# Kernel optimization log

Hardware: AMD Instinct MI355X
Metric: run time of the kernel (lower is better)

The kernel has to match this reference:

```python
import jax, jax.numpy as jnp
import numpy as np

# Sizes derived from init_kwargs via calc_mlp_features:
# total_param=2117777, router_ratio=0.002 -> router_param=4235.554, expert_param=264192
# expert_hidden = 256, router_hidden = 352
N = 131072      # number of coordinate points
CIN = 3         # expert_insize == router_insize (xyz coords)
E = 8           # num_experts
K = 2           # top_k
H = 256         # expert_hidden (also SIREN data_channel)
RH = 352        # router_hidden
NHID = 3        # expert_layers - 2 hidden SIREN layers
W0C = 30.0      # sine frequency w0


def setup_inputs() -> dict:
    key = jax.random.key(0)
    ks = jax.random.split(key, 16)
    u = lambda k, shape, a: jax.random.uniform(k, shape, jnp.float32, -a, a)
    x = jax.random.uniform(ks[0], (N, CIN), jnp.float32, -1.0, 1.0)
    context = jax.random.uniform(ks[1], (N, CIN), jnp.float32, -1.0, 1.0)
    # Router: kaiming-normal weights, torch-default uniform biases
    Wr1 = jax.random.normal(ks[2], (CIN, RH), jnp.float32) * np.float32(np.sqrt(2.0 / CIN))
    br1 = u(ks[3], (RH,), 1.0 / np.sqrt(CIN))
    Wr2 = jax.random.normal(ks[4], (RH, E), jnp.float32) * np.float32(np.sqrt(2.0 / RH))
    br2 = u(ks[5], (E,), 1.0 / np.sqrt(RH))
    # SIREN experts (stacked over E): first layer U(-1/in, 1/in), rest U(+-sqrt(6/in)/30)
    sb = np.sqrt(6.0 / H) / 30.0
    W0 = u(ks[6], (E, CIN, H), 1.0 / CIN)
    b0 = u(ks[7], (E, H), 1.0 / np.sqrt(CIN))
    Wh = u(ks[8], (E, NHID, H, H), sb)
    bh = u(ks[9], (E, NHID, H), 1.0 / np.sqrt(H))
    Wo = u(ks[10], (E, H, H), sb)
    bo = u(ks[11], (E, H), 1.0 / np.sqrt(H))
    # Decoder: Linear(H,H)+ReLU+Linear(H,1)
    Wd1 = jax.random.normal(ks[12], (H, H), jnp.float32) * np.float32(np.sqrt(2.0 / H))
    bd1 = u(ks[13], (H,), 1.0 / np.sqrt(H))
    Wd2 = jax.random.normal(ks[14], (H, 1), jnp.float32) * np.float32(np.sqrt(2.0 / H))
    bd2 = u(ks[15], (1,), 1.0 / np.sqrt(H))
    return dict(x=x, context=context, Wr1=Wr1, br1=br1, Wr2=Wr2, br2=br2,
                W0=W0, b0=b0, Wh=Wh, bh=bh, Wo=Wo, bo=bo,
                Wd1=Wd1, bd1=bd1, Wd2=Wd2, bd2=bd2)


def reference(x, context, Wr1, br1, Wr2, br2, W0, b0, Wh, bh, Wo, bo, Wd1, bd1, Wd2, bd2):
    n = x.shape[0]
    # --- NoisyTopkRouter (eval path: no noise) ---
    logits = jnp.maximum(context @ Wr1 + br1, 0.0) @ Wr2 + br2          # [N, E]
    topv, topi = jax.lax.top_k(logits, K)                                # [N, K]
    # softmax over -inf-filled sparse logits == softmax over the top-k values
    w = jax.nn.softmax(topv, axis=-1)                                    # [N, K]
    gating = jnp.zeros_like(logits).at[jnp.arange(n)[:, None], topi].set(w)  # [N, E], zero off top-k
    # --- Per-expert SIREN, weighted combine ---
    # Masked dispatch + scatter-add in the original equals dense weighted sum
    # because gating is exactly zero for non-selected experts.
    def expert_step(acc, p):
        W0e, b0e, Whe, bhe, Woe, boe, ge = p
        h = jnp.sin(W0C * (x @ W0e + b0e))                # [N, H]
        for i in range(NHID):
            h = jnp.sin(W0C * (h @ Whe[i] + bhe[i]))
        out = h @ Woe + boe                               # [N, H], no output activation
        return acc + out * ge[:, None], None
    acc0 = jnp.zeros((n, H), dtype=x.dtype)
    final, _ = jax.lax.scan(expert_step, acc0, (W0, b0, Wh, bh, Wo, bo, gating.T))
    # --- Decoder ---
    return jnp.maximum(final @ Wd1 + bd1, 0.0) @ Wd2 + bd2               # [N, 1]
```

## Files before the change

kernel.cpp:

```cpp
#include <hip/hip_runtime.h>
#include <stdint.h>

#define N_PTS 131072
#define RH    352
#define BM    256
#define BME   128
#define TPB   512
#define SREV  4.774648292756860f

typedef short  bf16x8 __attribute__((ext_vector_type(8)));
typedef float  f32x16 __attribute__((ext_vector_type(16)));

__device__ __forceinline__ unsigned short f2bf(float f) {
  uint32_t u = __builtin_bit_cast(uint32_t, f);
  u = (u + 0x7FFFu + ((u >> 16) & 1u)) >> 16;
  return (unsigned short)u;
}
__device__ __forceinline__ float bf2f(unsigned short s) {
  return __builtin_bit_cast(float, ((uint32_t)s) << 16);
}
__device__ __forceinline__ float vsin1(float x) {
  float xf = x - floorf(x);
  float r;
  asm("v_sin_f32 %0, %1" : "=v"(r) : "v"(xf));
  return r;
}
__device__ __forceinline__ void ldsload16(const void* g, void* ldsWaveBase) {
  typedef __attribute__((address_space(3))) uint8_t lds_b;
  typedef __attribute__((address_space(1))) uint8_t glob_b;
  __builtin_amdgcn_global_load_lds((const glob_b*)g, (lds_b*)ldsWaveBase, 16, 0, 0);
}
__device__ __forceinline__ f32x16 mfma_bf16(bf16x8 a, bf16x8 b, f32x16 c) {
  return __builtin_amdgcn_mfma_f32_32x32x16_bf16(a, b, c, 0, 0, 0);
}

__global__ __launch_bounds__(512) void pack_kernel(
    const float* __restrict__ W0, const float* __restrict__ b0,
    const float* __restrict__ Wh, const float* __restrict__ bh,
    const float* __restrict__ Wo, const float* __restrict__ bo,
    const float* __restrict__ Wd1, const float* __restrict__ bd1,
    short* __restrict__ pW0, short* __restrict__ pWh,
    short* __restrict__ pWo, short* __restrict__ pWd1)
{
  int b = blockIdx.x, tid = threadIdx.x;
  int jb = tid >> 6, l = tid & 63;
  int j  = jb*32 + (l & 31);
  int s0 = (l >> 5) * 8;
  unsigned short o[8];
  short* dp;

  if (b < 544) {
    int m = b / 17, slice = b % 17;
    int e = m >> 2, t = m & 3;
    const float* src; const float* bias; float scale; short* dst;
    if (t < 3) { src = Wh + (size_t)(e*3+t)*65536; bias = bh + (size_t)(e*3+t)*256; scale = SREV; dst = pWh + (size_t)(e*3+t)*69632; }
    else       { src = Wo + (size_t)e*65536;       bias = bo + (size_t)e*256;       scale = 1.0f; dst = pWo + (size_t)e*69632; }
    if (slice < 16) {
      #pragma unroll
      for (int i = 0; i < 8; ++i) {
        int k = slice*16 + s0 + i;
        o[i] = f2bf(scale * src[(size_t)k*256 + j]);
      }
    } else {
      #pragma unroll
      for (int i = 0; i < 8; ++i) o[i] = 0;
      if (s0 == 0) {
        float a = scale * bias[j];
        unsigned short h = f2bf(a);
        o[0] = h; o[1] = f2bf(a - bf2f(h));
      }
    }
    dp = dst + (size_t)slice*4096 + jb*512 + l*8;
  } else if (b < 552) {
    int e = b - 544;
    const float* w0 = W0 + (size_t)e*768;
    const float* bb = b0 + (size_t)e*256;
    #pragma unroll
    for (int i = 0; i < 8; ++i) {
      int s = s0 + i;
      unsigned short v = 0;
      if (s < 3) v = f2bf(SREV * w0[(size_t)s*256 + j]);
      else if (s < 6) { float a = SREV * w0[(size_t)(s-3)*256 + j]; unsigned short h = f2bf(a); v = f2bf(a - bf2f(h)); }
      else if (s < 9) v = f2bf(SREV * w0[(size_t)(s-6)*256 + j]);
      else if (s == 9)  v = f2bf(SREV * bb[j]);
      else if (s == 10) { float a = SREV * bb[j]; unsigned short h = f2bf(a); v = f2bf(a - bf2f(h)); }
      o[i] = v;
    }
    dp = pW0 + (size_t)e*4096 + jb*512 + l*8;
  } else {
    int slice = b - 552;
    if (slice < 16) {
      #pragma unroll
      for (int i = 0; i < 8; ++i) {
        int k = slice*16 + s0 + i;
        o[i] = f2bf(Wd1[(size_t)k*256 + j]);
      }
    } else {
      #pragma unroll
      for (int i = 0; i < 8; ++i) o[i] = 0;
      if (s0 == 0) {
        float a = bd1[j];
        unsigned short h = f2bf(a);
        o[0] = h; o[1] = f2bf(a - bf2f(h));
      }
    }
    dp = pWd1 + (size_t)slice*4096 + jb*512 + l*8;
  }
  uint4 v;
  v.x = (uint32_t)o[0] | ((uint32_t)o[1] << 16);
  v.y = (uint32_t)o[2] | ((uint32_t)o[3] << 16);
  v.z = (uint32_t)o[4] | ((uint32_t)o[5] << 16);
  v.w = (uint32_t)o[6] | ((uint32_t)o[7] << 16);
  *(uint4*)dp = v;
}

__global__ __launch_bounds__(256) void router_kernel(
    const float* __restrict__ ctx, const float* __restrict__ Wr1,
    const float* __restrict__ br1, const float* __restrict__ Wr2,
    const float* __restrict__ br2, uint4* __restrict__ topk,
    uint32_t* __restrict__ counts)
{
  __shared__ double w1d[RH*4];
  __shared__ double w2d[RH*8];
  __shared__ uint32_t lcnt[8];
  int tid = threadIdx.x;
  for (int i = tid; i < RH; i += 256) {
    w1d[i*4+0] = (double)Wr1[i];
    w1d[i*4+1] = (double)Wr1[352 + i];
    w1d[i*4+2] = (double)Wr1[704 + i];
    w1d[i*4+3] = (double)br1[i];
  }
  for (int i = tid; i < RH*8; i += 256) w2d[i] = (double)Wr2[i];
  if (tid < 8) lcnt[tid] = 0;
  __syncthreads();

  int n = blockIdx.x*256 + tid;
  double c0 = (double)ctx[(size_t)n*3+0];
  double c1 = (double)ctx[(size_t)n*3+1];
  double c2 = (double)ctx[(size_t)n*3+2];
  double lg[8];
  #pragma unroll
  for (int e = 0; e < 8; ++e) lg[e] = (double)br2[e];
  for (int j = 0; j < RH; ++j) {
    const double* a = &w1d[j*4];
    double h = c0*a[0] + c1*a[1] + c2*a[2] + a[3];
    h = h > 0.0 ? h : 0.0;
    const double* bq = &w2d[j*8];
    lg[0] += h*bq[0]; lg[1] += h*bq[1]; lg[2] += h*bq[2]; lg[3] += h*bq[3];
    lg[4] += h*bq[4]; lg[5] += h*bq[5]; lg[6] += h*bq[6]; lg[7] += h*bq[7];
  }
  double v0 = -1e300, v1 = -1e300; int i0 = 0, i1 = 0;
  #pragma unroll
  for (int e = 0; e < 8; ++e) {
    double lv = lg[e];
    if (lv > v0)      { v1 = v0; i1 = i0; v0 = lv; i0 = e; }
    else if (lv > v1) { v1 = lv; i1 = e; }
  }
  float ex = __expf((float)(v1 - v0));
  float s = 1.0f / (1.0f + ex);
  uint4 t;
  t.x = (uint32_t)i0 | ((uint32_t)i1 << 8);
  t.y = __builtin_bit_cast(uint32_t, s);
  t.z = __builtin_bit_cast(uint32_t, ex * s);
  t.w = 0;
  topk[n] = t;
  atomicAdd(&lcnt[i0], 1u); atomicAdd(&lcnt[i1], 1u);
  __syncthreads();
  if (tid < 8) atomicAdd(&counts[tid], lcnt[tid]);
}

__global__ void scan_kernel(const uint32_t* __restrict__ counts,
                            uint32_t* __restrict__ offsets,
                            uint32_t* __restrict__ cursors)
{
  if (threadIdx.x == 0) {
    uint32_t o = 0;
    for (int e = 0; e < 8; ++e) { offsets[e] = o; cursors[e] = o; o += counts[e]; }
    offsets[8] = o;
  }
}

__global__ __launch_bounds__(256) void scatter_kernel(
    const uint4* __restrict__ topk, uint32_t* __restrict__ cursors,
    uint32_t* __restrict__ plist, float* __restrict__ pw)
{
  __shared__ uint32_t lc[8], lb[8];
  int tid = threadIdx.x;
  if (tid < 8) lc[tid] = 0;
  __syncthreads();
  int n = blockIdx.x*256 + tid;
  uint4 t = topk[n];
  uint32_t e0 = t.x & 255u, e1 = (t.x >> 8) & 255u;
  uint32_t p0 = atomicAdd(&lc[e0], 1u);
  uint32_t p1 = atomicAdd(&lc[e1], 1u);
  __syncthreads();
  if (tid < 8) lb[tid] = atomicAdd(&cursors[tid], lc[tid]);
  __syncthreads();
  uint32_t d0 = lb[e0] + p0, d1 = lb[e1] + p1;
  plist[d0] = ((uint32_t)n << 1);      pw[d0] = __builtin_bit_cast(float, t.y);
  plist[d1] = ((uint32_t)n << 1) | 1u; pw[d1] = __builtin_bit_cast(float, t.z);
}

#define LDS_EXPERT 81920

__global__ __launch_bounds__(TPB, 4) void expert_kernel(
    const float* __restrict__ x, const uint32_t* __restrict__ counts,
    const uint32_t* __restrict__ offsets, const uint32_t* __restrict__ plist,
    const float* __restrict__ pw, const short* __restrict__ pW0,
    const short* __restrict__ pWh, const short* __restrict__ pWo,
    short* __restrict__ outbuf)
{
  extern __shared__ __align__(16) uint8_t smem[];
  uint8_t* hB = smem;
  uint8_t* wB = smem + 65536;

  int tid = threadIdx.x;
  int lane = tid & 63;
  int wv = tid >> 6;
  int nw = wv & 1;
  int jw = wv >> 1;

  int b = blockIdx.x;
  int e = 0; uint32_t cnt = 0;
  for (; e < 8; ++e) {
    cnt = counts[e];
    int nt = (int)((cnt + (BME-1)) / BME);
    if (b < nt) break;
    b -= nt;
  }
  if (e >= 8) return;
  uint32_t base = offsets[e] + (uint32_t)b * BME;
  int nvalid = (int)cnt - b*BME; if (nvalid > BME) nvalid = BME;

  float wgt[2];
  #pragma unroll
  for (int c = 0; c < 2; ++c) {
    int n = (nw*2 + c)*32 + (lane & 31);
    wgt[c] = (n < nvalid) ? pw[base + n] : 0.0f;
  }
  int rr = tid >> 2;
  int rq = tid & 3;
  uint32_t psv = (rr < nvalid) ? plist[base + rr] : 0u;

  ldsload16((const uint8_t*)(pW0 + (size_t)e*4096) + (size_t)tid*16,
            wB + wv*1024);
  if (tid < BME) {
    float x0 = 0.0f, x1 = 0.0f, x2 = 0.0f;
    if (tid < nvalid) {
      uint32_t v = plist[base + tid];
      const float* xp = x + (size_t)(v >> 1)*3;
      x0 = xp[0]; x1 = xp[1]; x2 = xp[2];
    }
    unsigned short h0 = f2bf(x0), h1 = f2bf(x1), h2 = f2bf(x2);
    unsigned short l0 = f2bf(x0 - bf2f(h0)), l1 = f2bf(x1 - bf2f(h1)), l2 = f2bf(x2 - bf2f(h2));
    uint4 r0, r1;
    r0.x = (uint32_t)h0 | ((uint32_t)h1 << 16);
    r0.y = (uint32_t)h2 | ((uint32_t)h0 << 16);
    r0.z = (uint32_t)h1 | ((uint32_t)h2 << 16);
    r0.w = (uint32_t)l0 | ((uint32_t)l1 << 16);
    r1.x = (uint32_t)l2 | (0x3F80u << 16);
    r1.y = 0x3F80u;
    r1.z = 0u; r1.w = 0u;
    uint4* dst = (uint4*)(wB + 8192 + tid*32);
    dst[0] = r0; dst[1] = r1;
  }
  __syncthreads();

  f32x16 acc[2][2];
  #pragma unroll
  for (int a2 = 0; a2 < 2; ++a2)
    #pragma unroll
    for (int c = 0; c < 2; ++c)
      #pragma unroll
      for (int r = 0; r < 16; ++r) acc[a2][c][r] = 0.0f;

  {
    bf16x8 av[2], bv[2];
    #pragma unroll
    for (int a2 = 0; a2 < 2; ++a2)
      av[a2] = *(const bf16x8*)(wB + (jw*2 + a2)*1024 + lane*16);
    #pragma unroll
    for (int c = 0; c < 2; ++c) {
      int n = (nw*2 + c)*32 + (lane & 31);
      bv[c] = *(const bf16x8*)(wB + 8192 + n*32 + ((lane >> 5)*16));
    }
    #pragma unroll
    for (int a2 = 0; a2 < 2; ++a2)
      #pragma unroll
      for (int c = 0; c < 2; ++c)
        acc[a2][c] = mfma_bf16(av[a2], bv[c], acc[a2][c]);
  }
  __syncthreads();

  #pragma unroll
  for (int a2 = 0; a2 < 2; ++a2) {
    int jb = jw*2 + a2;
    #pragma unroll
    for (int c = 0; c < 2; ++c) {
      int n = (nw*2 + c)*32 + (lane & 31);
      uint32_t rowb = (uint32_t)n * 512u;
      uint32_t sw = (uint32_t)((n & 7) << 4);
      #pragma unroll
      for (int g = 0; g < 4; ++g) {
        float s0f = vsin1(acc[a2][c][g*4+0]);
        float s1f = vsin1(acc[a2][c][g*4+1]);
        float s2f = vsin1(acc[a2][c][g*4+2]);
        float s3f = vsin1(acc[a2][c][g*4+3]);
        uint2 pv;
        pv.x = (uint32_t)f2bf(s0f) | ((uint32_t)f2bf(s1f) << 16);
        pv.y = (uint32_t)f2bf(s2f) | ((uint32_t)f2bf(s3f) << 16);
        int j0 = jb*32 + g*8 + ((lane >> 5) << 2);
        uint32_t off = (rowb + (uint32_t)(j0*2)) ^ sw;
        *(uint2*)(hB + off) = pv;
      }
    }
  }
  ldsload16((const uint8_t*)(pWh + (size_t)e*3*69632) + (size_t)tid*16,
            wB + wv*1024);
  __syncthreads();

  const short* mats[4];
  mats[0] = pWh + (size_t)(e*3+0)*69632;
  mats[1] = pWh + (size_t)(e*3+1)*69632;
  mats[2] = pWh + (size_t)(e*3+2)*69632;
  mats[3] = pWo + (size_t)e*69632;

  bf16x8 bbias;
  #pragma unroll
  for (int i = 0; i < 8; ++i) bbias[i] = 0;
  if (lane < 32) { bbias[0] = (short)0x3F80; bbias[1] = (short)0x3F80; }

  #pragma unroll 1
  for (int L = 0; L < 4; ++L) {
    const short* Wsrc = mats[L];
    #pragma unroll
    for (int a2 = 0; a2 < 2; ++a2)
      #pragma unroll
      for (int c = 0; c < 2; ++c)
        #pragma unroll
        for (int r = 0; r < 16; ++r) acc[a2][c][r] = 0.0f;
    #pragma unroll 1
    for (int kb = 0; kb < 17; ++kb) {
      if (kb < 16)
        ldsload16((const uint8_t*)(Wsrc + (size_t)(kb+1)*4096) + (size_t)tid*16,
                  wB + ((kb+1) & 1)*8192 + wv*1024);
      const uint8_t* wcur = wB + (kb & 1)*8192;
      bf16x8 av[2];
      #pragma unroll
      for (int a2 = 0; a2 < 2; ++a2)
        av[a2] = *(const bf16x8*)(wcur + (jw*2 + a2)*1024 + lane*16);
      bf16x8 bv[2];
      if (kb < 16) {
        #pragma unroll
        for (int c = 0; c < 2; ++c) {
          int n = (nw*2 + c)*32 + (lane & 31);
          uint32_t off = ((uint32_t)n*512u + (uint32_t)kb*32u + (uint32_t)((lane >> 5)*16))
                         ^ (uint32_t)((n & 7) << 4);
          bv[c] = *(const bf16x8*)(hB + off);
        }
      } else {
        bv[0] = bbias; bv[1] = bbias;
      }
      #pragma unroll
      for (int a2 = 0; a2 < 2; ++a2)
        #pragma unroll
        for (int c = 0; c < 2; ++c)
          acc[a2][c] = mfma_bf16(av[a2], bv[c], acc[a2][c]);
      __syncthreads();
    }
    if (L < 3) {
      #pragma unroll
      for (int a2 = 0; a2 < 2; ++a2) {
        int jb = jw*2 + a2;
        #pragma unroll
        for (int c = 0; c < 2; ++c) {
          int n = (nw*2 + c)*32 + (lane & 31);
          uint32_t rowb = (uint32_t)n * 512u;
          uint32_t sw = (uint32_t)((n & 7) << 4);
          #pragma unroll
          for (int g = 0; g < 4; ++g) {
            float s0f = vsin1(acc[a2][c][g*4+0]);
            float s1f = vsin1(acc[a2][c][g*4+1]);
            float s2f = vsin1(acc[a2][c][g*4+2]);
            float s3f = vsin1(acc[a2][c][g*4+3]);
            uint2 pv;
            pv.x = (uint32_t)f2bf(s0f) | ((uint32_t)f2bf(s1f) << 16);
            pv.y = (uint32_t)f2bf(s2f) | ((uint32_t)f2bf(s3f) << 16);
            int j0 = jb*32 + g*8 + ((lane >> 5) << 2);
            uint32_t off = (rowb + (uint32_t)(j0*2)) ^ sw;
            *(uint2*)(hB + off) = pv;
          }
        }
      }
      ldsload16((const uint8_t*)mats[L+1] + (size_t)tid*16, wB + wv*1024);
      __syncthreads();
    }
  }

  #pragma unroll
  for (int a2 = 0; a2 < 2; ++a2) {
    int jb = jw*2 + a2;
    #pragma unroll
    for (int c = 0; c < 2; ++c) {
      int n = (nw*2 + c)*32 + (lane & 31);
      float w = wgt[c];
      uint32_t rowb = (uint32_t)n * 512u;
      uint32_t sw = (uint32_t)((n & 7) << 4);
      #pragma unroll
      for (int g = 0; g < 4; ++g) {
        float s0f = acc[a2][c][g*4+0] * w;
        float s1f = acc[a2][c][g*4+1] * w;
        float s2f = acc[a2][c][g*4+2] * w;
        float s3f = acc[a2][c][g*4+3] * w;
        uint2 pv;
        pv.x = (uint32_t)f2bf(s0f) | ((uint32_t)f2bf(s1f) << 16);
        pv.y = (uint32_t)f2bf(s2f) | ((uint32_t)f2bf(s3f) << 16);
        int j0 = jb*32 + g*8 + ((lane >> 5) << 2);
        uint32_t off = (rowb + (uint32_t)(j0*2)) ^ sw;
        *(uint2*)(hB + off) = pv;
      }
    }
  }
  __syncthreads();
  if (rr < nvalid) {
    uint4* dst = (uint4*)(outbuf + ((size_t)(psv & 1)*N_PTS + (size_t)(psv >> 1))*256 + rq*64);
    uint32_t rowb = (uint32_t)rr*512u + (uint32_t)rq*128u;
    uint32_t sw = (uint32_t)((rr & 7) << 4);
    #pragma unroll
    for (int c = 0; c < 8; ++c)
      dst[c] = *(const uint4*)(hB + ((rowb + (uint32_t)c*16u) ^ sw));
  }
}

#define LDS_DEC 150528

__global__ __launch_bounds__(TPB, 2) void decoder_kernel(
    const short* __restrict__ outbuf, const short* __restrict__ pWd1,
    const float* __restrict__ Wd2v, const float* __restrict__ bd2,
    float* __restrict__ outp)
{
  extern __shared__ __align__(16) uint8_t smem[];
  uint8_t* hB = smem;
  uint8_t* wB = smem + 131072;
  float* wd2 = (float*)(smem + 147456);
  float* part = (float*)(smem + 148480);

  int tid = threadIdx.x;
  int lane = tid & 63;
  int wv = tid >> 6;
  int nw = wv & 3;
  int jw = wv >> 2;
  int tbase = blockIdx.x * BM;

  ldsload16((const uint8_t*)pWd1 + (size_t)tid*16, wB + (tid >> 6)*1024);
  if (tid < 256) wd2[tid] = Wd2v[tid];

  const short* o0 = outbuf + (size_t)tbase*256;
  const short* o1 = outbuf + ((size_t)N_PTS + tbase)*256;
  #pragma unroll 1
  for (int it = 0; it < 16; ++it) {
    int c = it*512 + tid;
    uint4 a  = *(const uint4*)(o0 + (size_t)c*8);
    uint4 bq = *(const uint4*)(o1 + (size_t)c*8);
    uint4 ov;
    uint32_t* ap = (uint32_t*)&a;
    uint32_t* bp = (uint32_t*)&bq;
    uint32_t* op = (uint32_t*)&ov;
    #pragma unroll
    for (int w = 0; w < 4; ++w) {
      uint32_t ua = ap[w], ub = bp[w];
      float f0 = bf2f((unsigned short)(ua & 0xFFFFu)) + bf2f((unsigned short)(ub & 0xFFFFu));
      float f1 = bf2f((unsigned short)(ua >> 16))     + bf2f((unsigned short)(ub >> 16));
      op[w] = (uint32_t)f2bf(f0) | ((uint32_t)f2bf(f1) << 16);
    }
    int n = c >> 5;
    uint32_t off = ((uint32_t)n*512u + (uint32_t)(c & 31)*16u) ^ (uint32_t)((n & 7) << 4);
    *(uint4*)(hB + off) = ov;
  }
  __syncthreads();

  f32x16 acc[4][2];
  #pragma unroll
  for (int a2 = 0; a2 < 4; ++a2)
    #pragma unroll
    for (int c = 0; c < 2; ++c)
      #pragma unroll
      for (int r = 0; r < 16; ++r) acc[a2][c][r] = 0.0f;
  bf16x8 bbias;
  #pragma unroll
  for (int i = 0; i < 8; ++i) bbias[i] = 0;
  if (lane < 32) { bbias[0] = (short)0x3F80; bbias[1] = (short)0x3F80; }

  #pragma unroll 1
  for (int kb = 0; kb < 17; ++kb) {
    if (kb < 16)
      ldsload16((const uint8_t*)(pWd1 + (size_t)(kb+1)*4096) + (size_t)tid*16,
                wB + ((kb+1) & 1)*8192 + (tid >> 6)*1024);
    const uint8_t* wcur = wB + (kb & 1)*8192;
    bf16x8 av[4];
    #pragma unroll
    for (int a2 = 0; a2 < 4; ++a2)
      av[a2] = *(const bf16x8*)(wcur + (jw*4 + a2)*1024 + lane*16);
    bf16x8 bv[2];
    if (kb < 16) {
      #pragma unroll
      for (int c = 0; c < 2; ++c) {
        int n = (nw*2 + c)*32 + (lane & 31);
        uint32_t off = ((uint32_t)n*512u + (uint32_t)kb*32u + (uint32_t)((lane >> 5)*16))
                       ^ (uint32_t)((n & 7) << 4);
        bv[c] = *(const bf16x8*)(hB + off);
      }
    } else {
      bv[0] = bbias; bv[1] = bbias;
    }
    #pragma unroll
    for (int a2 = 0; a2 < 4; ++a2)
      #pragma unroll
      for (int c = 0; c < 2; ++c)
        acc[a2][c] = mfma_bf16(av[a2], bv[c], acc[a2][c]);
    __syncthreads();
  }

  float p0 = 0.0f, p1 = 0.0f;
  #pragma unroll
  for (int a2 = 0; a2 < 4; ++a2) {
    int jb = jw*4 + a2;
    #pragma unroll
    for (int c = 0; c < 2; ++c) {
      #pragma unroll
      for (int r = 0; r < 16; ++r) {
        int j = jb*32 + (r & 3) + ((r >> 2) << 3) + ((lane >> 5) << 2);
        float v = acc[a2][c][r];
        v = v > 0.0f ? v : 0.0f;
        float t = v * wd2[j];
        if (c == 0) p0 += t; else p1 += t;
      }
    }
  }
  p0 += __shfl_xor(p0, 32);
  p1 += __shfl_xor(p1, 32);
  if (lane < 32) {
    part[jw*256 + (nw*2+0)*32 + lane] = p0;
    part[jw*256 + (nw*2+1)*32 + lane] = p1;
  }
  __syncthreads();
  if (tid < 256)
    outp[tbase + tid] = part[tid] + part[256 + tid] + bd2[0];
}

extern "C" void kernel_launch(void* const* d_in, const int* in_sizes, int n_in,
                              void* d_out, int out_size, void* d_ws, size_t ws_size,
                              hipStream_t stream) {
  const float* x   = (const float*)d_in[0];
  const float* ctx = (const float*)d_in[1];
  const float* Wr1 = (const float*)d_in[2];
  const float* br1 = (const float*)d_in[3];
  const float* Wr2 = (const float*)d_in[4];
  const float* br2 = (const float*)d_in[5];
  const float* W0  = (const float*)d_in[6];
  const float* b0  = (const float*)d_in[7];
  const float* Wh  = (const float*)d_in[8];
  const float* bh  = (const float*)d_in[9];
  const float* Wo  = (const float*)d_in[10];
  const float* bo  = (const float*)d_in[11];
  const float* Wd1 = (const float*)d_in[12];
  const float* bd1 = (const float*)d_in[13];
  const float* Wd2 = (const float*)d_in[14];
  const float* bd2 = (const float*)d_in[15];
  float* out = (float*)d_out;

  const size_t WS_COUNTS  = 0;
  const size_t WS_CURSORS = 256;
  const size_t WS_OFFSETS = 512;
  const size_t WS_TOPK    = 1024;
  const size_t WS_PLIST   = WS_TOPK  + (size_t)N_PTS*16;
  const size_t WS_PW      = WS_PLIST + (size_t)N_PTS*8;
  const size_t WS_PW0     = WS_PW    + (size_t)N_PTS*8;
  const size_t WS_PWH     = WS_PW0   + (size_t)8*8192;
  const size_t WS_PWO     = WS_PWH   + (size_t)24*139264;
  const size_t WS_PWD1    = WS_PWO   + (size_t)8*139264;
  const size_t WS_OUT     = WS_PWD1  + (size_t)139264;
  const size_t WS_END     = WS_OUT   + (size_t)2*N_PTS*256*2;

  if (ws_size < WS_END) {
    hipMemsetAsync(d_out, 0xFF, (size_t)out_size*4, stream);
    return;
  }

  uint8_t* ws = (uint8_t*)d_ws;
  uint32_t* counts  = (uint32_t*)(ws + WS_COUNTS);
  uint32_t* cursors = (uint32_t*)(ws + WS_CURSORS);
  uint32_t* offsets = (uint32_t*)(ws + WS_OFFSETS);
  uint4*    topk    = (uint4*)   (ws + WS_TOPK);
  uint32_t* plist   = (uint32_t*)(ws + WS_PLIST);
  float*    pw      = (float*)   (ws + WS_PW);
  short*    pW0     = (short*)   (ws + WS_PW0);
  short*    pWh     = (short*)   (ws + WS_PWH);
  short*    pWo     = (short*)   (ws + WS_PWO);
  short*    pWd1    = (short*)   (ws + WS_PWD1);
  short*    outbuf  = (short*)   (ws + WS_OUT);

  hipMemsetAsync(counts, 0, 32, stream);
  hipFuncSetAttribute((const void*)expert_kernel,
                      hipFuncAttributeMaxDynamicSharedMemorySize, LDS_EXPERT);
  hipFuncSetAttribute((const void*)decoder_kernel,
                      hipFuncAttributeMaxDynamicSharedMemorySize, LDS_DEC);

  pack_kernel   <<<569,  512, 0, stream>>>(W0, b0, Wh, bh, Wo, bo, Wd1, bd1,
                                           pW0, pWh, pWo, pWd1);
  router_kernel <<<512,  256, 0, stream>>>(ctx, Wr1, br1, Wr2, br2, topk, counts);
  scan_kernel   <<<1,     64, 0, stream>>>(counts, offsets, cursors);
  scatter_kernel<<<512,  256, 0, stream>>>(topk, cursors, plist, pw);
  expert_kernel <<<2056, TPB, LDS_EXPERT, stream>>>(x, counts, offsets, plist, pw,
                                                    pW0, pWh, pWo, outbuf);
  decoder_kernel<<<512,  TPB, LDS_DEC, stream>>>(outbuf, pWd1, Wd2, bd2, out);
}
```

Before: 333.8 us.

## Hold expert weights in registers and shrink expert tile to 64 points

The expert kernel now has each of 4 waves keep its full 256x272 weight slice (17 k-steps) in registers, loaded straight from global memory. This replaces the double-buffered LDS weight staging and the barrier after every k-step. The point tile drops from 128 to 64 and the block from 512 to 256 threads, with static LDS of about 34 KB and twice as many blocks. The next layer's weights are prefetched into registers during the current layer. The costs are very high register pressure (34 bf16x8 operands plus accumulators, with possible spills or lower occupancy) and each block rereading the weights from global or L2 memory with half the point reuse.

Result: slower. 541.5 us (+62.2%).

```diff
diff --git a/kernel.cpp b/kernel.cpp
--- a/kernel.cpp
+++ b/kernel.cpp
@@ -4,7 +4,7 @@
 #define N_PTS 131072
 #define RH    352
 #define BM    256
-#define BME   128
+#define BME   64
 #define TPB   512
 #define SREV  4.774648292756860f
 
@@ -201,49 +201,43 @@
   plist[d1] = ((uint32_t)n << 1) | 1u; pw[d1] = __builtin_bit_cast(float, t.z);
 }
 
-#define LDS_EXPERT 81920
-
-__global__ __launch_bounds__(TPB, 4) void expert_kernel(
+__global__ __launch_bounds__(256, 2) void expert_kernel(
     const float* __restrict__ x, const uint32_t* __restrict__ counts,
     const uint32_t* __restrict__ offsets, const uint32_t* __restrict__ plist,
     const float* __restrict__ pw, const short* __restrict__ pW0,
     const short* __restrict__ pWh, const short* __restrict__ pWo,
     short* __restrict__ outbuf)
 {
-  extern __shared__ __align__(16) uint8_t smem[];
+  __shared__ __align__(16) uint8_t smem[34816];
   uint8_t* hB = smem;
-  uint8_t* wB = smem + 65536;
+  uint8_t* xB = smem + 32768;
 
   int tid = threadIdx.x;
   int lane = tid & 63;
-  int wv = tid >> 6;
-  int nw = wv & 1;
-  int jw = wv >> 1;
+  int jw = tid >> 6;
 
   int b = blockIdx.x;
   int e = 0; uint32_t cnt = 0;
   for (; e < 8; ++e) {
     cnt = counts[e];
-    int nt = (int)((cnt + (BME-1)) / BME);
+    int nt = (int)((cnt + (BME-1)) >> 6);
     if (b < nt) break;
     b -= nt;
   }
   if (e >= 8) return;
-  uint32_t base = offsets[e] + (uint32_t)b * BME;
-  int nvalid = (int)cnt - b*BME; if (nvalid > BME) nvalid = BME;
+  uint32_t base = offsets[e] + ((uint32_t)b << 6);
+  int nvalid = (int)cnt - (b << 6); if (nvalid > BME) nvalid = BME;
 
   float wgt[2];
   #pragma unroll
   for (int c = 0; c < 2; ++c) {
-    int n = (nw*2 + c)*32 + (lane & 31);
+    int n = c*32 + (lane & 31);
     wgt[c] = (n < nvalid) ? pw[base + n] : 0.0f;
   }
   int rr = tid >> 2;
   int rq = tid & 3;
   uint32_t psv = (rr < nvalid) ? plist[base + rr] : 0u;
 
-  ldsload16((const uint8_t*)(pW0 + (size_t)e*4096) + (size_t)tid*16,
-            wB + wv*1024);
   if (tid < BME) {
     float x0 = 0.0f, x1 = 0.0f, x2 = 0.0f;
     if (tid < nvalid) {
@@ -261,9 +255,16 @@
     r1.x = (uint32_t)l2 | (0x3F80u << 16);
     r1.y = 0x3F80u;
     r1.z = 0u; r1.w = 0u;
-    uint4* dst = (uint4*)(wB + 8192 + tid*32);
+    uint4* dst = (uint4*)(xB + tid*32);
     dst[0] = r0; dst[1] = r1;
   }
+
+  const uint8_t* pw0e = (const uint8_t*)(pW0 + (size_t)e*4096);
+  bf16x8 a0[2];
+  #pragma unroll
+  for (int a2 = 0; a2 < 2; ++a2)
+    a0[a2] = *(const bf16x8*)(pw0e + (jw*2 + a2)*1024 + lane*16);
+
   __syncthreads();
 
   f32x16 acc[2][2];
@@ -275,29 +276,25 @@
       for (int r = 0; r < 16; ++r) acc[a2][c][r] = 0.0f;
 
   {
-    bf16x8 av[2], bv[2];
+    bf16x8 bv[2];
+    #pragma unroll
+    for (int c = 0; c < 2; ++c) {
+      int n = c*32 + (lane & 31);
+      bv[c] = *(const bf16x8*)(xB + n*32 + ((lane >> 5)*16));
+    }
     #pragma unroll
     for (int a2 = 0; a2 < 2; ++a2)
-      av[a2] = *(const bf16x8*)(wB + (jw*2 + a2)*1024 + lane*16);
-    #pragma unroll
-    for (int c = 0; c < 2; ++c) {
-      int n = (nw*2 + c)*32 + (lane & 31);
-      bv[c] = *(const bf16x8*)(wB + 8192 + n*32 + ((lane >> 5)*16));
-    }
-    #pragma unroll
-    for (int a2 = 0; a2 < 2; ++a2)
       #pragma unroll
       for (int c = 0; c < 2; ++c)
-        acc[a2][c] = mfma_bf16(av[a2], bv[c], acc[a2][c]);
-  }
-  __syncthreads();
+        acc[a2][c] = mfma_bf16(a0[a2], bv[c], acc[a2][c]);
+  }
 
   #pragma unroll
   for (int a2 = 0; a2 < 2; ++a2) {
     int jb = jw*2 + a2;
     #pragma unroll
     for (int c = 0; c < 2; ++c) {
-      int n = (nw*2 + c)*32 + (lane & 31);
+      int n = c*32 + (lane & 31);
       uint32_t rowb = (uint32_t)n * 512u;
       uint32_t sw = (uint32_t)((n & 7) << 4);
       #pragma unroll
@@ -315,9 +312,6 @@
       }
     }
   }
-  ldsload16((const uint8_t*)(pWh + (size_t)e*3*69632) + (size_t)tid*16,
-            wB + wv*1024);
-  __syncthreads();
 
   const short* mats[4];
   mats[0] = pWh + (size_t)(e*3+0)*69632;
@@ -325,56 +319,72 @@
   mats[2] = pWh + (size_t)(e*3+2)*69632;
   mats[3] = pWo + (size_t)e*69632;
 
+  bf16x8 aw[17][2];
+  {
+    const uint8_t* wb0 = (const uint8_t*)mats[0];
+    #pragma unroll
+    for (int s = 0; s < 17; ++s)
+      #pragma unroll
+      for (int a2 = 0; a2 < 2; ++a2)
+        aw[s][a2] = *(const bf16x8*)(wb0 + (size_t)s*8192 + (jw*2 + a2)*1024 + lane*16);
+  }
+
   bf16x8 bbias;
   #pragma unroll
   for (int i = 0; i < 8; ++i) bbias[i] = 0;
   if (lane < 32) { bbias[0] = (short)0x3F80; bbias[1] = (short)0x3F80; }
 
-  #pragma unroll 1
+  __syncthreads();
+
+  #pragma unroll
   for (int L = 0; L < 4; ++L) {
-    const short* Wsrc = mats[L];
     #pragma unroll
     for (int a2 = 0; a2 < 2; ++a2)
       #pragma unroll
       for (int c = 0; c < 2; ++c)
         #pragma unroll
         for (int r = 0; r < 16; ++r) acc[a2][c][r] = 0.0f;
-    #pragma unroll 1
-    for (int kb = 0; kb < 17; ++kb) {
-      if (kb < 16)
-        ldsload16((const uint8_t*)(Wsrc + (size_t)(kb+1)*4096) + (size_t)tid*16,
-                  wB + ((kb+1) & 1)*8192 + wv*1024);
-      const uint8_t* wcur = wB + (kb & 1)*8192;
-      bf16x8 av[2];
-      #pragma unroll
-      for (int a2 = 0; a2 < 2; ++a2)
-        av[a2] = *(const bf16x8*)(wcur + (jw*2 + a2)*1024 + lane*16);
+
+    #pragma unroll
+    for (int kb = 0; kb < 16; ++kb) {
       bf16x8 bv[2];
-      if (kb < 16) {
-        #pragma unroll
-        for (int c = 0; c < 2; ++c) {
-          int n = (nw*2 + c)*32 + (lane & 31);
-          uint32_t off = ((uint32_t)n*512u + (uint32_t)kb*32u + (uint32_t)((lane >> 5)*16))
-                         ^ (uint32_t)((n & 7) << 4);
-          bv[c] = *(const bf16x8*)(hB + off);
-        }
-      } else {
-        bv[0] = bbias; bv[1] = bbias;
+      #pragma unroll
+      for (int c = 0; c < 2; ++c) {
+        int n = c*32 + (lane & 31);
+        uint32_t off = ((uint32_t)n*512u + (uint32_t)(kb*32) + (uint32_t)((lane >> 5)*16))
+                       ^ (uint32_t)((n & 7) << 4);
+        bv[c] = *(const bf16x8*)(hB + off);
       }
       #pragma unroll
       for (int a2 = 0; a2 < 2; ++a2)
         #pragma unroll
         for (int c = 0; c < 2; ++c)
-          acc[a2][c] = mfma_bf16(av[a2], bv[c], acc[a2][c]);
-      __syncthreads();
-    }
+          acc[a2][c] = mfma_bf16(aw[kb][a2], bv[c], acc[a2][c]);
+    }
+    #pragma unroll
+    for (int a2 = 0; a2 < 2; ++a2)
+      #pragma unroll
+      for (int c = 0; c < 2; ++c)
+        acc[a2][c] = mfma_bf16(aw[16][a2], bbias, acc[a2][c]);
+
+    if (L < 3) {
+      const uint8_t* wbn = (const uint8_t*)mats[L+1];
+      #pragma unroll
+      for (int s = 0; s < 17; ++s)
+        #pragma unroll
+        for (int a2 = 0; a2 < 2; ++a2)
+          aw[s][a2] = *(const bf16x8*)(wbn + (size_t)s*8192 + (jw*2 + a2)*1024 + lane*16);
+    }
+
+    __syncthreads();
+
     if (L < 3) {
       #pragma unroll
       for (int a2 = 0; a2 < 2; ++a2) {
         int jb = jw*2 + a2;
         #pragma unroll
         for (int c = 0; c < 2; ++c) {
-          int n = (nw*2 + c)*32 + (lane & 31);
+          int n = c*32 + (lane & 31);
           uint32_t rowb = (uint32_t)n * 512u;
           uint32_t sw = (uint32_t)((n & 7) << 4);
           #pragma unroll
@@ -392,36 +402,35 @@
           }
         }
       }
-      ldsload16((const uint8_t*)mats[L+1] + (size_t)tid*16, wB + wv*1024);
-      __syncthreads();
-    }
-  }
-
-  #pragma unroll
-  for (int a2 = 0; a2 < 2; ++a2) {
-    int jb = jw*2 + a2;
-    #pragma unroll
-    for (int c = 0; c < 2; ++c) {
-      int n = (nw*2 + c)*32 + (lane & 31);
-      float w = wgt[c];
-      uint32_t rowb = (uint32_t)n * 512u;
-      uint32_t sw = (uint32_t)((n & 7) << 4);
-      #pragma unroll
-      for (int g = 0; g < 4; ++g) {
-        float s0f = acc[a2][c][g*4+0] * w;
-        float s1f = acc[a2][c][g*4+1] * w;
-        float s2f = acc[a2][c][g*4+2] * w;
-        float s3f = acc[a2][c][g*4+3] * w;
-        uint2 pv;
-        pv.x = (uint32_t)f2bf(s0f) | ((uint32_t)f2bf(s1f) << 16);
-        pv.y = (uint32_t)f2bf(s2f) | ((uint32_t)f2bf(s3f) << 16);
-        int j0 = jb*32 + g*8 + ((lane >> 5) << 2);
-        uint32_t off = (rowb + (uint32_t)(j0*2)) ^ sw;
-        *(uint2*)(hB + off) = pv;
-      }
-    }
-  }
-  __syncthreads();
+    } else {
+      #pragma unroll
+      for (int a2 = 0; a2 < 2; ++a2) {
+        int jb = jw*2 + a2;
+        #pragma unroll
+        for (int c = 0; c < 2; ++c) {
+          int n = c*32 + (lane & 31);
+          float w = wgt[c];
+          uint32_t rowb = (uint32_t)n * 512u;
+          uint32_t sw = (uint32_t)((n & 7) << 4);
+          #pragma unroll
+          for (int g = 0; g < 4; ++g) {
+            float s0f = acc[a2][c][g*4+0] * w;
+            float s1f = acc[a2][c][g*4+1] * w;
+            float s2f = acc[a2][c][g*4+2] * w;
+            float s3f = acc[a2][c][g*4+3] * w;
+            uint2 pv;
+            pv.x = (uint32_t)f2bf(s0f) | ((uint32_t)f2bf(s1f) << 16);
+            pv.y = (uint32_t)f2bf(s2f) | ((uint32_t)f2bf(s3f) << 16);
+            int j0 = jb*32 + g*8 + ((lane >> 5) << 2);
+            uint32_t off = (rowb + (uint32_t)(j0*2)) ^ sw;
+            *(uint2*)(hB + off) = pv;
+          }
+        }
+      }
+    }
+    __syncthreads();
+  }
+
   if (rr < nvalid) {
     uint4* dst = (uint4*)(outbuf + ((size_t)(psv & 1)*N_PTS + (size_t)(psv >> 1))*256 + rq*64);
     uint32_t rowb = (uint32_t)rr*512u + (uint32_t)rq*128u;
@@ -601,8 +610,6 @@
   short*    outbuf  = (short*)   (ws + WS_OUT);
 
   hipMemsetAsync(counts, 0, 32, stream);
-  hipFuncSetAttribute((const void*)expert_kernel,
-                      hipFuncAttributeMaxDynamicSharedMemorySize, LDS_EXPERT);
   hipFuncSetAttribute((const void*)decoder_kernel,
                       hipFuncAttributeMaxDynamicSharedMemorySize, LDS_DEC);
 
@@ -611,7 +618,7 @@
   router_kernel <<<512,  256, 0, stream>>>(ctx, Wr1, br1, Wr2, br2, topk, counts);
   scan_kernel   <<<1,     64, 0, stream>>>(counts, offsets, cursors);
   scatter_kernel<<<512,  256, 0, stream>>>(topk, cursors, plist, pw);
-  expert_kernel <<<2056, TPB, LDS_EXPERT, stream>>>(x, counts, offsets, plist, pw,
-                                                    pW0, pWh, pWo, outbuf);
+  expert_kernel <<<4104,  256, 0, stream>>>(x, counts, offsets, plist, pw,
+                                            pW0, pWh, pWo, outbuf);
   decoder_kernel<<<512,  TPB, LDS_DEC, stream>>>(outbuf, pWd1, Wd2, bd2, out);
 }
```
